# Kernel optimization log

Measured on AMD Instinct MI355X. Metric: run time of the kernel, lower is better.

Reference implementation:

```python
import jax, jax.numpy as jnp
import numpy as np

N_NODES = 50000


def gcn_conv(x, W, b, src, dst, n_nodes):
    # PyG GCNConv: h = D^{-1/2}(A+I)D^{-1/2} X W + b, with self-loops added.
    h = x @ W                                   # [N, H]
    loops = jnp.arange(n_nodes, dtype=src.dtype)
    s = jnp.concatenate([src, loops])           # [E+N]
    d = jnp.concatenate([dst, loops])
    deg = jax.ops.segment_sum(jnp.ones_like(d, dtype=h.dtype), d, num_segments=n_nodes)
    dinv = jnp.where(deg > 0, jax.lax.rsqrt(deg), 0.0)
    norm = dinv[s] * dinv[d]                    # [E+N]
    msg = h[s] * norm[:, None]                  # gather + scale
    agg = jax.ops.segment_sum(msg, d, num_segments=n_nodes)  # scatter-add
    return agg + b


def setup_inputs() -> dict:
    key = jax.random.key(0)
    ks = jax.random.split(key, 8)
    N, E, D, H, ED = N_NODES, 800000, 64, 64, 16
    sc = lambda f_in: 1.0 / np.sqrt(f_in)
    return {
        "x": jax.random.normal(ks[0], (N, D), dtype=jnp.float32),
        "src": jax.random.randint(ks[1], (E,), 0, N),
        "dst": jax.random.randint(ks[2], (E,), 0, N),
        "edge_attr": jax.random.normal(ks[3], (E, ED), dtype=jnp.float32),
        "W1": jax.random.normal(ks[4], (D, H), dtype=jnp.float32) * sc(D),
        "b1": jnp.zeros((H,), dtype=jnp.float32),
        "Wm1": jax.random.normal(ks[5], (2 * H + ED, H), dtype=jnp.float32) * sc(2 * H + ED),
        "bm1": jnp.zeros((H,), dtype=jnp.float32),
        "Wm2": jax.random.normal(ks[6], (H, 1), dtype=jnp.float32) * sc(H),
        "bm2": jnp.zeros((1,), dtype=jnp.float32),
    }


def reference(x, src, dst, edge_attr, W1, b1, Wm1, bm1, Wm2, bm2):
    h = jax.nn.relu(gcn_conv(x, W1, b1, src, dst, N_NODES))  # [N, H]
    edge_repr = jnp.concatenate([h[src], h[dst], edge_attr], axis=1)  # [E, 2H+ED]
    hidden = jax.nn.relu(edge_repr @ Wm1 + bm1)
    scores = jax.nn.sigmoid(hidden @ Wm2 + bm2)
    return scores.squeeze(-1)
```

## Files before the change

kernel.cpp:

```cpp
#include <hip/hip_runtime.h>
#include <math.h>


typedef __attribute__((ext_vector_type(8))) short bf16x8;
typedef __attribute__((ext_vector_type(4))) float f32x4;

#define MAXDEG 64
#define BSHIFT 7
#define BMASK 127
#define NBUCK 391
#define CAP 2560
#define CHUNK 4096
#define BINB 196
#define BPB 40

__device__ __forceinline__ unsigned short f2b(float f) {
    unsigned u = __float_as_uint(f);
    unsigned r = (u + 0x7FFFu + ((u >> 16) & 1u)) >> 16;
    return (unsigned short)r;
}

__global__ void __launch_bounds__(256) bin_pack(
        const int* __restrict__ dst, const int* __restrict__ src,
        unsigned int* __restrict__ region, int* __restrict__ gcur, int E,
        const float* __restrict__ Wm1, unsigned short* __restrict__ Bp) {
    __shared__ __align__(16) char smem[32768];
    const int bid = blockIdx.x, tid = threadIdx.x;

    if (bid < BINB) {
        int* lc = (int*)smem;
        int* s0 = lc + 512;
        int* s1 = s0 + 512;
        int* gb = s1 + 512;
        unsigned* lval = (unsigned*)(gb + 512);
        unsigned short* lbuk = (unsigned short*)(lval + 4096);

        for (int i = tid; i < 512; i += 256) lc[i] = 0;
        __syncthreads();

        unsigned kb[16], kv[16];
#pragma unroll
        for (int j = 0; j < 4; ++j) {
            int i4 = bid * 1024 + j * 256 + tid;
            bool ok = (i4 * 4 < E);
            int4 d4 = make_int4(0, 0, 0, 0), s4 = make_int4(0, 0, 0, 0);
            if (ok) { d4 = ((const int4*)dst)[i4]; s4 = ((const int4*)src)[i4]; }
            int dd[4] = {d4.x, d4.y, d4.z, d4.w};
            int ss[4] = {s4.x, s4.y, s4.z, s4.w};
#pragma unroll
            for (int k = 0; k < 4; ++k) {
                int idx = j * 4 + k;
                kb[idx] = 0xFFFFFFFFu;
                if (ok) {
                    int b = dd[k] >> BSHIFT;
                    int r = atomicAdd(&lc[b], 1);
                    kb[idx] = ((unsigned)b << 12) | (unsigned)r;
                    kv[idx] = ((unsigned)(dd[k] & BMASK) << 16) | (unsigned)ss[k];
                }
            }
        }
        __syncthreads();

        for (int i = tid; i < 512; i += 256) s0[i] = lc[i];
        __syncthreads();
        int* pin = s0; int* pout = s1;
        for (int off = 1; off < 512; off <<= 1) {
            for (int i = tid; i < 512; i += 256) {
                int v = pin[i];
                if (i >= off) v += pin[i - off];
                pout[i] = v;
            }
            __syncthreads();
            int* t = pin; pin = pout; pout = t;
        }
        int* lb = pout;
        for (int i = tid; i < 512; i += 256) lb[i] = pin[i] - lc[i];
        for (int i = tid; i < NBUCK; i += 256) {
            int c = lc[i];
            gb[i] = c ? atomicAdd(&gcur[i], c) : 0;
        }
        __syncthreads();

#pragma unroll
        for (int idx = 0; idx < 16; ++idx) {
            if (kb[idx] != 0xFFFFFFFFu) {
                int b = (int)(kb[idx] >> 12), r = (int)(kb[idx] & 4095u);
                int pos = lb[b] + r;
                lval[pos] = kv[idx];
                lbuk[pos] = (unsigned short)b;
            }
        }
        __syncthreads();

        int ne = E - bid * CHUNK; if (ne > CHUNK) ne = CHUNK;
        for (int i = tid; i < ne; i += 256) {
            int b = lbuk[i];
            int idx = gb[b] + (i - lb[b]);
            if (idx < CAP) region[(size_t)b * CAP + idx] = lval[i];
        }
    } else {
        int idx = (bid - BINB) * 256 + tid;
        if (idx < 10240) {
            int j = idx & 7, ln = (idx >> 3) & 63, t = (idx >> 9) & 3, s = idx >> 11;
            int k = s * 32 + (ln >> 4) * 8 + j, col = t * 16 + (ln & 15);
            float v = (k < 144) ? Wm1[k * 64 + col] : 0.0f;
            Bp[idx] = f2b(v);
        }
    }
}

__global__ void __launch_bounds__(256) build_csr(
        const unsigned int* __restrict__ region, const int* __restrict__ gcur,
        int* __restrict__ cnt, unsigned short* __restrict__ csr_pad, int N) {
    __shared__ unsigned short lcsr[128 * MAXDEG];
    __shared__ int lcnt[128];
    int b = blockIdx.x, tid = threadIdx.x;
    if (tid < 128) lcnt[tid] = 0;
    __syncthreads();
    int ecnt = gcur[b]; if (ecnt > CAP) ecnt = CAP;
    const unsigned int* reg = region + (size_t)b * CAP;
    for (int i = tid; i < ecnt; i += 256) {
        unsigned v = reg[i];
        int dloc = (int)(v >> 16), s = (int)(v & 0xFFFFu);
        int r = atomicAdd(&lcnt[dloc], 1);
        if (r < MAXDEG) lcsr[dloc * MAXDEG + r] = (unsigned short)s;
    }
    __syncthreads();
    int n0 = b << BSHIFT;
    int nb = N - n0; if (nb > 128) nb = 128;
    if (tid < nb) cnt[n0 + tid] = lcnt[tid];
    int4* gout = (int4*)(csr_pad + (size_t)n0 * MAXDEG);
    const int4* lin = (const int4*)lcsr;
    int tot = nb * 8;
    for (int i = tid; i < tot; i += 256) gout[i] = lin[i];
}

__global__ void __launch_bounds__(256) node_gemm_mfma(
        const float* __restrict__ x, const float* __restrict__ W1,
        const int* __restrict__ cnt, unsigned short* __restrict__ gbf, int NWT) {
    __shared__ unsigned short sB[4096];
    for (int i = threadIdx.x; i < 4096; i += 256) {
        int j = i & 7, ln = (i >> 3) & 63, t = (i >> 9) & 3, s = i >> 11;
        int k = s * 32 + (ln >> 4) * 8 + j, col = t * 16 + (ln & 15);
        sB[i] = f2b(W1[k * 64 + col]);
    }
    __syncthreads();
    int wid = blockIdx.x * 4 + (threadIdx.x >> 6);
    if (wid >= NWT) return;
    int lane = threadIdx.x & 63, m = lane & 15, quad = lane >> 4;
    int r0 = wid * 16;
    f32x4 acc[4];
#pragma unroll
    for (int t = 0; t < 4; ++t) acc[t] = (f32x4){0.f, 0.f, 0.f, 0.f};
    const bf16x8* bp = (const bf16x8*)sB;
#pragma unroll
    for (int s = 0; s < 2; ++s) {
        const float4* xp = (const float4*)(x + (size_t)(r0 + m) * 64 + s * 32 + quad * 8);
        float4 v0 = xp[0], v1 = xp[1];
        bf16x8 a;
        a[0] = (short)f2b(v0.x); a[1] = (short)f2b(v0.y);
        a[2] = (short)f2b(v0.z); a[3] = (short)f2b(v0.w);
        a[4] = (short)f2b(v1.x); a[5] = (short)f2b(v1.y);
        a[6] = (short)f2b(v1.z); a[7] = (short)f2b(v1.w);
#pragma unroll
        for (int t = 0; t < 4; ++t)
            acc[t] = __builtin_amdgcn_mfma_f32_16x16x32_bf16(
                a, bp[(s * 4 + t) * 64 + lane], acc[t], 0, 0, 0);
    }
#pragma unroll
    for (int reg = 0; reg < 4; ++reg) {
        int row = r0 + quad * 4 + reg;
        float di = rsqrtf((float)cnt[row] + 1.0f);
#pragma unroll
        for (int t = 0; t < 4; ++t)
            gbf[(size_t)row * 64 + t * 16 + m] = f2b(acc[t][reg] * di);
    }
}

#define ACC8(U) \
    a0 += __uint_as_float((unsigned)(U).x << 16); \
    a1 += __uint_as_float((unsigned)(U).x & 0xffff0000u); \
    a2 += __uint_as_float((unsigned)(U).y << 16); \
    a3 += __uint_as_float((unsigned)(U).y & 0xffff0000u); \
    a4 += __uint_as_float((unsigned)(U).z << 16); \
    a5 += __uint_as_float((unsigned)(U).z & 0xffff0000u); \
    a6 += __uint_as_float((unsigned)(U).w << 16); \
    a7 += __uint_as_float((unsigned)(U).w & 0xffff0000u);

__global__ void __launch_bounds__(256) gather_finalize(
        const unsigned short* __restrict__ gbf, const unsigned short* __restrict__ csr_pad,
        const int* __restrict__ cnt, const float* __restrict__ b1,
        unsigned short* __restrict__ hbf, int N) {
    int t = blockIdx.x * 256 + threadIdx.x;
    int node = t >> 3;
    if (node >= N) return;
    int c8 = t & 7;
    int deg = cnt[node];
    if (deg > MAXDEG) deg = MAXDEG;
    size_t base = (size_t)node << 6;
    const int4* gb4 = (const int4*)gbf;
    float a0 = 0.f, a1 = 0.f, a2 = 0.f, a3 = 0.f,
          a4 = 0.f, a5 = 0.f, a6 = 0.f, a7 = 0.f;
    int j = 0;
    for (; j + 4 <= deg; j += 4) {
        int s0 = (int)csr_pad[base + j];
        int s1 = (int)csr_pad[base + j + 1];
        int s2 = (int)csr_pad[base + j + 2];
        int s3 = (int)csr_pad[base + j + 3];
        int4 u0 = gb4[(size_t)s0 * 8 + c8];
        int4 u1 = gb4[(size_t)s1 * 8 + c8];
        int4 u2 = gb4[(size_t)s2 * 8 + c8];
        int4 u3 = gb4[(size_t)s3 * 8 + c8];
        ACC8(u0) ACC8(u1) ACC8(u2) ACC8(u3)
    }
    for (; j < deg; ++j) {
        int s0 = (int)csr_pad[base + j];
        int4 u0 = gb4[(size_t)s0 * 8 + c8];
        ACC8(u0)
    }
    {
        int4 u = gb4[(size_t)node * 8 + c8];
        ACC8(u)
    }
    float dd = rsqrtf((float)deg + 1.0f);
    const float4* bv = (const float4*)(b1 + c8 * 8);
    float4 b0 = bv[0], b14 = bv[1];
    float h0 = dd * a0 + b0.x,  h1 = dd * a1 + b0.y;
    float h2 = dd * a2 + b0.z,  h3 = dd * a3 + b0.w;
    float h4 = dd * a4 + b14.x, h5 = dd * a5 + b14.y;
    float h6 = dd * a6 + b14.z, h7 = dd * a7 + b14.w;
    h0 = h0 > 0.f ? h0 : 0.f; h1 = h1 > 0.f ? h1 : 0.f;
    h2 = h2 > 0.f ? h2 : 0.f; h3 = h3 > 0.f ? h3 : 0.f;
    h4 = h4 > 0.f ? h4 : 0.f; h5 = h5 > 0.f ? h5 : 0.f;
    h6 = h6 > 0.f ? h6 : 0.f; h7 = h7 > 0.f ? h7 : 0.f;
    int4 w;
    w.x = (int)((unsigned)f2b(h0) | ((unsigned)f2b(h1) << 16));
    w.y = (int)((unsigned)f2b(h2) | ((unsigned)f2b(h3) << 16));
    w.z = (int)((unsigned)f2b(h4) | ((unsigned)f2b(h5) << 16));
    w.w = (int)((unsigned)f2b(h6) | ((unsigned)f2b(h7) << 16));
    ((int4*)hbf)[(size_t)node * 8 + c8] = w;
}

__global__ void __launch_bounds__(256, 8) edge_mlp_mfma(
        const unsigned short* __restrict__ hbf, const float* __restrict__ ea,
        const int* __restrict__ src, const int* __restrict__ dst,
        const unsigned short* __restrict__ Bp,
        const float* __restrict__ bm1, const float* __restrict__ Wm2,
        const float* __restrict__ bm2, float* __restrict__ out, int E) {
    __shared__ unsigned short sB[10240];
    {
        const int4* gB = (const int4*)Bp;
        int4* lB = (int4*)sB;
#pragma unroll
        for (int i = 0; i < 5; ++i)
            lB[threadIdx.x + i * 256] = gB[threadIdx.x + i * 256];
    }
    __syncthreads();
    int lane = threadIdx.x & 63;
    int wave = threadIdx.x >> 6;
    int m = lane & 15, quad = lane >> 4;
    int e0 = (blockIdx.x * 4 + wave) * 16;
    if (e0 >= E) return;
    int e = e0 + m;
    int ec = e < E ? e : E - 1;
    int si = src[ec], di = dst[ec];
    bf16x8 af[5];
    af[0] = *(const bf16x8*)(hbf + (size_t)si * 64 + quad * 8);
    af[1] = *(const bf16x8*)(hbf + (size_t)si * 64 + 32 + quad * 8);
    af[2] = *(const bf16x8*)(hbf + (size_t)di * 64 + quad * 8);
    af[3] = *(const bf16x8*)(hbf + (size_t)di * 64 + 32 + quad * 8);
    if (quad < 2) {
        const float4* ep = (const float4*)(ea + (size_t)ec * 16 + quad * 8);
        float4 v0 = ep[0], v1 = ep[1];
        af[4][0] = (short)f2b(v0.x); af[4][1] = (short)f2b(v0.y);
        af[4][2] = (short)f2b(v0.z); af[4][3] = (short)f2b(v0.w);
        af[4][4] = (short)f2b(v1.x); af[4][5] = (short)f2b(v1.y);
        af[4][6] = (short)f2b(v1.z); af[4][7] = (short)f2b(v1.w);
    } else {
#pragma unroll
        for (int j = 0; j < 8; ++j) af[4][j] = 0;
    }
    __builtin_amdgcn_sched_barrier(0);
    f32x4 acc[4];
#pragma unroll
    for (int t = 0; t < 4; ++t) acc[t] = (f32x4){0.f, 0.f, 0.f, 0.f};
    const bf16x8* bp = (const bf16x8*)sB;
#pragma unroll
    for (int s = 0; s < 5; ++s) {
#pragma unroll
        for (int t = 0; t < 4; ++t)
            acc[t] = __builtin_amdgcn_mfma_f32_16x16x32_bf16(
                af[s], bp[(s * 4 + t) * 64 + lane], acc[t], 0, 0, 0);
    }
    float w2[4], bb[4];
#pragma unroll
    for (int t = 0; t < 4; ++t) {
        int col = t * 16 + m;
        bb[t] = bm1[col];
        w2[t] = Wm2[col];
    }
    float pr[4];
#pragma unroll
    for (int r = 0; r < 4; ++r) {
        float sum = 0.0f;
#pragma unroll
        for (int t = 0; t < 4; ++t) {
            float hv = acc[t][r] + bb[t];
            sum += (hv > 0.0f ? hv : 0.0f) * w2[t];
        }
        pr[r] = sum;
    }
#pragma unroll
    for (int off = 1; off < 16; off <<= 1) {
#pragma unroll
        for (int r = 0; r < 4; ++r) pr[r] += __shfl_xor(pr[r], off, 64);
    }
    float b2 = bm2[0];
    if (m < 4) {
        int eo = e0 + quad * 4 + m;
        if (eo < E) out[eo] = 1.0f / (1.0f + __expf(-(pr[m] + b2)));
    }
}

extern "C" void kernel_launch(void* const* d_in, const int* in_sizes, int n_in,
                              void* d_out, int out_size, void* d_ws, size_t ws_size,
                              hipStream_t stream) {
    const float* x   = (const float*)d_in[0];
    const int*   src = (const int*)d_in[1];
    const int*   dst = (const int*)d_in[2];
    const float* ea  = (const float*)d_in[3];
    const float* W1  = (const float*)d_in[4];
    const float* b1  = (const float*)d_in[5];
    const float* Wm1 = (const float*)d_in[6];
    const float* bm1 = (const float*)d_in[7];
    const float* Wm2 = (const float*)d_in[8];
    const float* bm2 = (const float*)d_in[9];
    float* out = (float*)d_out;

    int N = in_sizes[0] / 64;
    int E = in_sizes[1];
    int NWT = N / 16;

    char* p = (char*)d_ws;
    unsigned short* gbf     = (unsigned short*)p; p += (size_t)N * 64 * 2;
    unsigned short* hbf     = (unsigned short*)p; p += (size_t)N * 64 * 2;
    unsigned short* csr_pad = (unsigned short*)p; p += (size_t)N * MAXDEG * 2;
    int*            cnt     = (int*)p;            p += (size_t)N * 4;
    int*            gcur    = (int*)p;            p += (size_t)((NBUCK * 4 + 15) / 16) * 16;
    unsigned short* Bp      = (unsigned short*)p; p += 10240 * 2;
    unsigned int*   region  = (unsigned int*)hbf;

    hipMemsetAsync(gcur, 0, NBUCK * sizeof(int), stream);
    bin_pack<<<BINB + BPB, 256, 0, stream>>>(dst, src, region, gcur, E, Wm1, Bp);
    build_csr<<<NBUCK, 256, 0, stream>>>(region, gcur, cnt, csr_pad, N);
    node_gemm_mfma<<<(NWT + 3) / 4, 256, 0, stream>>>(x, W1, cnt, gbf, NWT);
    gather_finalize<<<(N * 8 + 255) / 256, 256, 0, stream>>>(gbf, csr_pad, cnt, b1, hbf, N);
    edge_mlp_mfma<<<(E + 63) / 64, 256, 0, stream>>>(hbf, ea, src, dst, Bp,
                                                     bm1, Wm2, bm2, out, E);
}
```

Before: 189.0 us.

## Drop CSR build; aggregate directly from bucketed edges via LDS atomics

Removes the build_csr kernel and padded CSR buffer. Degree counting moves into the node GEMM kernel, which reads bucket regions per 64-node half. Aggregation now runs one block per 128-node bucket and scatters gathered bf16 rows into a shared fp32 tile with LDS float atomics. bin_pack is also reconfigured with half-size chunks and twice the blocks. This saves one kernel launch and the CSR write/read, but adds many LDS atomics and a second pass over the region in gemm_cnt. It also drops the MAXDEG cap, which changes semantics for high-degree nodes, and region no longer aliases hbf.

```diff
diff --git a/kernel.cpp b/kernel.cpp
--- a/kernel.cpp
+++ b/kernel.cpp
@@ -10,9 +10,10 @@
 #define BMASK 127
 #define NBUCK 391
 #define CAP 2560
-#define CHUNK 4096
-#define BINB 196
+#define CHUNK 2048
+#define BINB 391
 #define BPB 40
+#define TSTR 68
 
 __device__ __forceinline__ unsigned short f2b(float f) {
     unsigned u = __float_as_uint(f);
@@ -24,7 +25,7 @@
         const int* __restrict__ dst, const int* __restrict__ src,
         unsigned int* __restrict__ region, int* __restrict__ gcur, int E,
         const float* __restrict__ Wm1, unsigned short* __restrict__ Bp) {
-    __shared__ __align__(16) char smem[32768];
+    __shared__ __align__(16) char smem[20480];
     const int bid = blockIdx.x, tid = threadIdx.x;
 
     if (bid < BINB) {
@@ -33,15 +34,15 @@
         int* s1 = s0 + 512;
         int* gb = s1 + 512;
         unsigned* lval = (unsigned*)(gb + 512);
-        unsigned short* lbuk = (unsigned short*)(lval + 4096);
+        unsigned short* lbuk = (unsigned short*)(lval + 2048);
 
         for (int i = tid; i < 512; i += 256) lc[i] = 0;
         __syncthreads();
 
-        unsigned kb[16], kv[16];
-#pragma unroll
-        for (int j = 0; j < 4; ++j) {
-            int i4 = bid * 1024 + j * 256 + tid;
+        unsigned kb[8], kv[8];
+#pragma unroll
+        for (int j = 0; j < 2; ++j) {
+            int i4 = bid * 512 + j * 256 + tid;
             bool ok = (i4 * 4 < E);
             int4 d4 = make_int4(0, 0, 0, 0), s4 = make_int4(0, 0, 0, 0);
             if (ok) { d4 = ((const int4*)dst)[i4]; s4 = ((const int4*)src)[i4]; }
@@ -82,7 +83,7 @@
         __syncthreads();
 
 #pragma unroll
-        for (int idx = 0; idx < 16; ++idx) {
+        for (int idx = 0; idx < 8; ++idx) {
             if (kb[idx] != 0xFFFFFFFFu) {
                 int b = (int)(kb[idx] >> 12), r = (int)(kb[idx] & 4095u);
                 int pos = lb[b] + r;
@@ -109,45 +110,35 @@
     }
 }
 
-__global__ void __launch_bounds__(256) build_csr(
+__global__ void __launch_bounds__(256) gemm_cnt(
+        const float* __restrict__ x, const float* __restrict__ W1,
         const unsigned int* __restrict__ region, const int* __restrict__ gcur,
-        int* __restrict__ cnt, unsigned short* __restrict__ csr_pad, int N) {
-    __shared__ unsigned short lcsr[128 * MAXDEG];
-    __shared__ int lcnt[128];
-    int b = blockIdx.x, tid = threadIdx.x;
-    if (tid < 128) lcnt[tid] = 0;
-    __syncthreads();
-    int ecnt = gcur[b]; if (ecnt > CAP) ecnt = CAP;
-    const unsigned int* reg = region + (size_t)b * CAP;
-    for (int i = tid; i < ecnt; i += 256) {
-        unsigned v = reg[i];
-        int dloc = (int)(v >> 16), s = (int)(v & 0xFFFFu);
-        int r = atomicAdd(&lcnt[dloc], 1);
-        if (r < MAXDEG) lcsr[dloc * MAXDEG + r] = (unsigned short)s;
-    }
-    __syncthreads();
-    int n0 = b << BSHIFT;
-    int nb = N - n0; if (nb > 128) nb = 128;
-    if (tid < nb) cnt[n0 + tid] = lcnt[tid];
-    int4* gout = (int4*)(csr_pad + (size_t)n0 * MAXDEG);
-    const int4* lin = (const int4*)lcsr;
-    int tot = nb * 8;
-    for (int i = tid; i < tot; i += 256) gout[i] = lin[i];
-}
-
-__global__ void __launch_bounds__(256) node_gemm_mfma(
-        const float* __restrict__ x, const float* __restrict__ W1,
-        const int* __restrict__ cnt, unsigned short* __restrict__ gbf, int NWT) {
+        unsigned short* __restrict__ gbf, int N) {
     __shared__ unsigned short sB[4096];
-    for (int i = threadIdx.x; i < 4096; i += 256) {
+    __shared__ int lcnt[64];
+    __shared__ float ldinv[64];
+    const int tid = threadIdx.x, bid = blockIdx.x;
+    for (int i = tid; i < 4096; i += 256) {
         int j = i & 7, ln = (i >> 3) & 63, t = (i >> 9) & 3, s = i >> 11;
         int k = s * 32 + (ln >> 4) * 8 + j, col = t * 16 + (ln & 15);
         sB[i] = f2b(W1[k * 64 + col]);
     }
-    __syncthreads();
-    int wid = blockIdx.x * 4 + (threadIdx.x >> 6);
+    if (tid < 64) lcnt[tid] = 0;
+    __syncthreads();
+    int bucket = bid >> 1, half = bid & 1;
+    int ecnt = gcur[bucket]; if (ecnt > CAP) ecnt = CAP;
+    const unsigned int* reg = region + (size_t)bucket * CAP;
+    for (int i = tid; i < ecnt; i += 256) {
+        int dloc = (int)(reg[i] >> 16);
+        if ((dloc >> 6) == half) atomicAdd(&lcnt[dloc & 63], 1);
+    }
+    __syncthreads();
+    if (tid < 64) ldinv[tid] = rsqrtf((float)lcnt[tid] + 1.0f);
+    __syncthreads();
+    int wid = bid * 4 + (tid >> 6);
+    int NWT = (N + 15) / 16;
     if (wid >= NWT) return;
-    int lane = threadIdx.x & 63, m = lane & 15, quad = lane >> 4;
+    int lane = tid & 63, m = lane & 15, quad = lane >> 4;
     int r0 = wid * 16;
     f32x4 acc[4];
 #pragma unroll
@@ -168,77 +159,84 @@
                 a, bp[(s * 4 + t) * 64 + lane], acc[t], 0, 0, 0);
     }
 #pragma unroll
-    for (int reg = 0; reg < 4; ++reg) {
-        int row = r0 + quad * 4 + reg;
-        float di = rsqrtf((float)cnt[row] + 1.0f);
+    for (int reg2 = 0; reg2 < 4; ++reg2) {
+        int row = r0 + quad * 4 + reg2;
+        float di = ldinv[row - bid * 64];
 #pragma unroll
         for (int t = 0; t < 4; ++t)
-            gbf[(size_t)row * 64 + t * 16 + m] = f2b(acc[t][reg] * di);
-    }
-}
-
-#define ACC8(U) \
-    a0 += __uint_as_float((unsigned)(U).x << 16); \
-    a1 += __uint_as_float((unsigned)(U).x & 0xffff0000u); \
-    a2 += __uint_as_float((unsigned)(U).y << 16); \
-    a3 += __uint_as_float((unsigned)(U).y & 0xffff0000u); \
-    a4 += __uint_as_float((unsigned)(U).z << 16); \
-    a5 += __uint_as_float((unsigned)(U).z & 0xffff0000u); \
-    a6 += __uint_as_float((unsigned)(U).w << 16); \
-    a7 += __uint_as_float((unsigned)(U).w & 0xffff0000u);
-
-__global__ void __launch_bounds__(256) gather_finalize(
-        const unsigned short* __restrict__ gbf, const unsigned short* __restrict__ csr_pad,
-        const int* __restrict__ cnt, const float* __restrict__ b1,
+            gbf[(size_t)row * 64 + t * 16 + m] = f2b(acc[t][reg2] * di);
+    }
+}
+
+__global__ void __launch_bounds__(256) aggregate_finalize(
+        const unsigned short* __restrict__ gbf, const unsigned int* __restrict__ region,
+        const int* __restrict__ gcur, const float* __restrict__ b1,
         unsigned short* __restrict__ hbf, int N) {
-    int t = blockIdx.x * 256 + threadIdx.x;
-    int node = t >> 3;
-    if (node >= N) return;
-    int c8 = t & 7;
-    int deg = cnt[node];
-    if (deg > MAXDEG) deg = MAXDEG;
-    size_t base = (size_t)node << 6;
+    __shared__ float tile[128 * TSTR];
+    __shared__ int lcnt[128];
+    const int tid = threadIdx.x, b = blockIdx.x;
+    {
+        float4* t4 = (float4*)tile;
+        for (int i = tid; i < 128 * TSTR / 4; i += 256)
+            t4[i] = make_float4(0.f, 0.f, 0.f, 0.f);
+    }
+    if (tid < 128) lcnt[tid] = 0;
+    __syncthreads();
+    int ecnt = gcur[b]; if (ecnt > CAP) ecnt = CAP;
+    const unsigned int* reg = region + (size_t)b * CAP;
     const int4* gb4 = (const int4*)gbf;
-    float a0 = 0.f, a1 = 0.f, a2 = 0.f, a3 = 0.f,
-          a4 = 0.f, a5 = 0.f, a6 = 0.f, a7 = 0.f;
-    int j = 0;
-    for (; j + 4 <= deg; j += 4) {
-        int s0 = (int)csr_pad[base + j];
-        int s1 = (int)csr_pad[base + j + 1];
-        int s2 = (int)csr_pad[base + j + 2];
-        int s3 = (int)csr_pad[base + j + 3];
-        int4 u0 = gb4[(size_t)s0 * 8 + c8];
-        int4 u1 = gb4[(size_t)s1 * 8 + c8];
-        int4 u2 = gb4[(size_t)s2 * 8 + c8];
-        int4 u3 = gb4[(size_t)s3 * 8 + c8];
-        ACC8(u0) ACC8(u1) ACC8(u2) ACC8(u3)
-    }
-    for (; j < deg; ++j) {
-        int s0 = (int)csr_pad[base + j];
-        int4 u0 = gb4[(size_t)s0 * 8 + c8];
-        ACC8(u0)
-    }
-    {
-        int4 u = gb4[(size_t)node * 8 + c8];
-        ACC8(u)
-    }
-    float dd = rsqrtf((float)deg + 1.0f);
-    const float4* bv = (const float4*)(b1 + c8 * 8);
-    float4 b0 = bv[0], b14 = bv[1];
-    float h0 = dd * a0 + b0.x,  h1 = dd * a1 + b0.y;
-    float h2 = dd * a2 + b0.z,  h3 = dd * a3 + b0.w;
-    float h4 = dd * a4 + b14.x, h5 = dd * a5 + b14.y;
-    float h6 = dd * a6 + b14.z, h7 = dd * a7 + b14.w;
-    h0 = h0 > 0.f ? h0 : 0.f; h1 = h1 > 0.f ? h1 : 0.f;
-    h2 = h2 > 0.f ? h2 : 0.f; h3 = h3 > 0.f ? h3 : 0.f;
-    h4 = h4 > 0.f ? h4 : 0.f; h5 = h5 > 0.f ? h5 : 0.f;
-    h6 = h6 > 0.f ? h6 : 0.f; h7 = h7 > 0.f ? h7 : 0.f;
-    int4 w;
-    w.x = (int)((unsigned)f2b(h0) | ((unsigned)f2b(h1) << 16));
-    w.y = (int)((unsigned)f2b(h2) | ((unsigned)f2b(h3) << 16));
-    w.z = (int)((unsigned)f2b(h4) | ((unsigned)f2b(h5) << 16));
-    w.w = (int)((unsigned)f2b(h6) | ((unsigned)f2b(h7) << 16));
-    ((int4*)hbf)[(size_t)node * 8 + c8] = w;
+    int ntask = ecnt * 8;
+    int c8 = tid & 7;
+    for (int i = tid; i < ntask; i += 256) {
+        int e = i >> 3;
+        unsigned v = reg[e];
+        int dloc = (int)(v >> 16), s = (int)(v & 0xFFFFu);
+        int4 u = gb4[(size_t)s * 8 + c8];
+        float* tr = &tile[dloc * TSTR + c8 * 8];
+        atomicAdd(&tr[0], __uint_as_float((unsigned)u.x << 16));
+        atomicAdd(&tr[1], __uint_as_float((unsigned)u.x & 0xffff0000u));
+        atomicAdd(&tr[2], __uint_as_float((unsigned)u.y << 16));
+        atomicAdd(&tr[3], __uint_as_float((unsigned)u.y & 0xffff0000u));
+        atomicAdd(&tr[4], __uint_as_float((unsigned)u.z << 16));
+        atomicAdd(&tr[5], __uint_as_float((unsigned)u.z & 0xffff0000u));
+        atomicAdd(&tr[6], __uint_as_float((unsigned)u.w << 16));
+        atomicAdd(&tr[7], __uint_as_float((unsigned)u.w & 0xffff0000u));
+        if (c8 == 0) atomicAdd(&lcnt[dloc], 1);
+    }
+    __syncthreads();
+    int n0 = b << BSHIFT;
+    int nb = N - n0; if (nb > 128) nb = 128;
+    for (int i = tid; i < nb * 8; i += 256) {
+        int dloc = i >> 3, cc = i & 7;
+        int node = n0 + dloc;
+        float dd = rsqrtf((float)lcnt[dloc] + 1.0f);
+        int4 u = gb4[(size_t)node * 8 + cc];
+        const float* tr = &tile[dloc * TSTR + cc * 8];
+        float a0 = tr[0] + __uint_as_float((unsigned)u.x << 16);
+        float a1 = tr[1] + __uint_as_float((unsigned)u.x & 0xffff0000u);
+        float a2 = tr[2] + __uint_as_float((unsigned)u.y << 16);
+        float a3 = tr[3] + __uint_as_float((unsigned)u.y & 0xffff0000u);
+        float a4 = tr[4] + __uint_as_float((unsigned)u.z << 16);
+        float a5 = tr[5] + __uint_as_float((unsigned)u.z & 0xffff0000u);
+        float a6 = tr[6] + __uint_as_float((unsigned)u.w << 16);
+        float a7 = tr[7] + __uint_as_float((unsigned)u.w & 0xffff0000u);
+        const float4* bv = (const float4*)(b1 + cc * 8);
+        float4 b0 = bv[0], b14 = bv[1];
+        float h0 = dd * a0 + b0.x,  h1 = dd * a1 + b0.y;
+        float h2 = dd * a2 + b0.z,  h3 = dd * a3 + b0.w;
+        float h4 = dd * a4 + b14.x, h5 = dd * a5 + b14.y;
+        float h6 = dd * a6 + b14.z, h7 = dd * a7 + b14.w;
+        h0 = h0 > 0.f ? h0 : 0.f; h1 = h1 > 0.f ? h1 : 0.f;
+        h2 = h2 > 0.f ? h2 : 0.f; h3 = h3 > 0.f ? h3 : 0.f;
+        h4 = h4 > 0.f ? h4 : 0.f; h5 = h5 > 0.f ? h5 : 0.f;
+        h6 = h6 > 0.f ? h6 : 0.f; h7 = h7 > 0.f ? h7 : 0.f;
+        int4 w;
+        w.x = (int)((unsigned)f2b(h0) | ((unsigned)f2b(h1) << 16));
+        w.y = (int)((unsigned)f2b(h2) | ((unsigned)f2b(h3) << 16));
+        w.z = (int)((unsigned)f2b(h4) | ((unsigned)f2b(h5) << 16));
+        w.w = (int)((unsigned)f2b(h6) | ((unsigned)f2b(h7) << 16));
+        ((int4*)hbf)[(size_t)node * 8 + cc] = w;
+    }
 }
 
 __global__ void __launch_bounds__(256, 8) edge_mlp_mfma(
@@ -339,22 +337,18 @@
 
     int N = in_sizes[0] / 64;
     int E = in_sizes[1];
-    int NWT = N / 16;
 
     char* p = (char*)d_ws;
-    unsigned short* gbf     = (unsigned short*)p; p += (size_t)N * 64 * 2;
-    unsigned short* hbf     = (unsigned short*)p; p += (size_t)N * 64 * 2;
-    unsigned short* csr_pad = (unsigned short*)p; p += (size_t)N * MAXDEG * 2;
-    int*            cnt     = (int*)p;            p += (size_t)N * 4;
-    int*            gcur    = (int*)p;            p += (size_t)((NBUCK * 4 + 15) / 16) * 16;
-    unsigned short* Bp      = (unsigned short*)p; p += 10240 * 2;
-    unsigned int*   region  = (unsigned int*)hbf;
+    unsigned short* gbf    = (unsigned short*)p; p += (size_t)N * 64 * 2;
+    unsigned short* hbf    = (unsigned short*)p; p += (size_t)N * 64 * 2;
+    unsigned int*   region = (unsigned int*)p;   p += (size_t)NBUCK * CAP * 4;
+    int*            gcur   = (int*)p;            p += (size_t)((NBUCK * 4 + 15) / 16) * 16;
+    unsigned short* Bp     = (unsigned short*)p; p += 10240 * 2;
 
     hipMemsetAsync(gcur, 0, NBUCK * sizeof(int), stream);
     bin_pack<<<BINB + BPB, 256, 0, stream>>>(dst, src, region, gcur, E, Wm1, Bp);
-    build_csr<<<NBUCK, 256, 0, stream>>>(region, gcur, cnt, csr_pad, N);
-    node_gemm_mfma<<<(NWT + 3) / 4, 256, 0, stream>>>(x, W1, cnt, gbf, NWT);
-    gather_finalize<<<(N * 8 + 255) / 256, 256, 0, stream>>>(gbf, csr_pad, cnt, b1, hbf, N);
+    gemm_cnt<<<(N + 63) / 64, 256, 0, stream>>>(x, W1, region, gcur, gbf, N);
+    aggregate_finalize<<<NBUCK, 256, 0, stream>>>(gbf, region, gcur, b1, hbf, N);
     edge_mlp_mfma<<<(E + 63) / 64, 256, 0, stream>>>(hbf, ea, src, dst, Bp,
                                                      bm1, Wm2, bm2, out, E);
 }
```

New measurement: 521.2 us. +175.7%, slower.

## Merge node GEMM into binning launch and defer degree scaling to CSR build

Applied to the files above, without the earlier changes.

The node X·W1 MFMA GEMM now runs as extra blocks inside the binning kernel, so it no longer needs the degree counts and no longer waits on its own launch. The D^-1/2 source scaling moves into the CSR build kernel, which rescales each bucket's 128 gbf rows in place once the counts are known. This drops one kernel launch and lets the GEMM overlap with edge binning. The cost is an extra read-modify-write pass over gbf and a second bf16 rounding of the scaled values.

```diff
diff --git a/kernel.cpp b/kernel.cpp
--- a/kernel.cpp
+++ b/kernel.cpp
@@ -12,6 +12,7 @@
 #define CAP 2560
 #define CHUNK 4096
 #define BINB 196
+#define GEMB 782
 #define BPB 40
 
 __device__ __forceinline__ unsigned short f2b(float f) {
@@ -20,10 +21,12 @@
     return (unsigned short)r;
 }
 
-__global__ void __launch_bounds__(256) bin_pack(
+__global__ void __launch_bounds__(256) bin_gemm_pack(
         const int* __restrict__ dst, const int* __restrict__ src,
         unsigned int* __restrict__ region, int* __restrict__ gcur, int E,
-        const float* __restrict__ Wm1, unsigned short* __restrict__ Bp) {
+        const float* __restrict__ x, const float* __restrict__ W1,
+        unsigned short* __restrict__ gbf,
+        const float* __restrict__ Wm1, unsigned short* __restrict__ Bp, int N) {
     __shared__ __align__(16) char smem[32768];
     const int bid = blockIdx.x, tid = threadIdx.x;
 
@@ -98,8 +101,47 @@
             int idx = gb[b] + (i - lb[b]);
             if (idx < CAP) region[(size_t)b * CAP + idx] = lval[i];
         }
+    } else if (bid < BINB + GEMB) {
+        unsigned short* sB = (unsigned short*)smem;
+        for (int i = tid; i < 4096; i += 256) {
+            int j = i & 7, ln = (i >> 3) & 63, t = (i >> 9) & 3, s = i >> 11;
+            int k = s * 32 + (ln >> 4) * 8 + j, col = t * 16 + (ln & 15);
+            sB[i] = f2b(W1[k * 64 + col]);
+        }
+        __syncthreads();
+        int wid = (bid - BINB) * 4 + (tid >> 6);
+        int NWT = N / 16;
+        if (wid < NWT) {
+            int lane = tid & 63, m = lane & 15, quad = lane >> 4;
+            int r0 = wid * 16;
+            f32x4 acc[4];
+#pragma unroll
+            for (int t = 0; t < 4; ++t) acc[t] = (f32x4){0.f, 0.f, 0.f, 0.f};
+            const bf16x8* bp = (const bf16x8*)sB;
+#pragma unroll
+            for (int s = 0; s < 2; ++s) {
+                const float4* xp = (const float4*)(x + (size_t)(r0 + m) * 64 + s * 32 + quad * 8);
+                float4 v0 = xp[0], v1 = xp[1];
+                bf16x8 a;
+                a[0] = (short)f2b(v0.x); a[1] = (short)f2b(v0.y);
+                a[2] = (short)f2b(v0.z); a[3] = (short)f2b(v0.w);
+                a[4] = (short)f2b(v1.x); a[5] = (short)f2b(v1.y);
+                a[6] = (short)f2b(v1.z); a[7] = (short)f2b(v1.w);
+#pragma unroll
+                for (int t = 0; t < 4; ++t)
+                    acc[t] = __builtin_amdgcn_mfma_f32_16x16x32_bf16(
+                        a, bp[(s * 4 + t) * 64 + lane], acc[t], 0, 0, 0);
+            }
+#pragma unroll
+            for (int reg = 0; reg < 4; ++reg) {
+                int row = r0 + quad * 4 + reg;
+#pragma unroll
+                for (int t = 0; t < 4; ++t)
+                    gbf[(size_t)row * 64 + t * 16 + m] = f2b(acc[t][reg]);
+            }
+        }
     } else {
-        int idx = (bid - BINB) * 256 + tid;
+        int idx = (bid - BINB - GEMB) * 256 + tid;
         if (idx < 10240) {
             int j = idx & 7, ln = (idx >> 3) & 63, t = (idx >> 9) & 3, s = idx >> 11;
             int k = s * 32 + (ln >> 4) * 8 + j, col = t * 16 + (ln & 15);
@@ -109,11 +151,13 @@
     }
 }
 
-__global__ void __launch_bounds__(256) build_csr(
+__global__ void __launch_bounds__(256) build_scale(
         const unsigned int* __restrict__ region, const int* __restrict__ gcur,
-        int* __restrict__ cnt, unsigned short* __restrict__ csr_pad, int N) {
+        int* __restrict__ cnt, unsigned short* __restrict__ csr_pad,
+        unsigned short* __restrict__ gbf, int N) {
     __shared__ unsigned short lcsr[128 * MAXDEG];
     __shared__ int lcnt[128];
+    __shared__ float ldinv[128];
     int b = blockIdx.x, tid = threadIdx.x;
     if (tid < 128) lcnt[tid] = 0;
     __syncthreads();
@@ -129,51 +173,32 @@
     int n0 = b << BSHIFT;
     int nb = N - n0; if (nb > 128) nb = 128;
     if (tid < nb) cnt[n0 + tid] = lcnt[tid];
-    int4* gout = (int4*)(csr_pad + (size_t)n0 * MAXDEG);
-    const int4* lin = (const int4*)lcsr;
-    int tot = nb * 8;
-    for (int i = tid; i < tot; i += 256) gout[i] = lin[i];
-}
-
-__global__ void __launch_bounds__(256) node_gemm_mfma(
-        const float* __restrict__ x, const float* __restrict__ W1,
-        const int* __restrict__ cnt, unsigned short* __restrict__ gbf, int NWT) {
-    __shared__ unsigned short sB[4096];
-    for (int i = threadIdx.x; i < 4096; i += 256) {
-        int j = i & 7, ln = (i >> 3) & 63, t = (i >> 9) & 3, s = i >> 11;
-        int k = s * 32 + (ln >> 4) * 8 + j, col = t * 16 + (ln & 15);
-        sB[i] = f2b(W1[k * 64 + col]);
+    if (tid < 128) ldinv[tid] = rsqrtf((float)lcnt[tid] + 1.0f);
+    {
+        int4* gout = (int4*)(csr_pad + (size_t)n0 * MAXDEG);
+        const int4* lin = (const int4*)lcsr;
+        int tot = nb * 8;
+        for (int i = tid; i < tot; i += 256) gout[i] = lin[i];
     }
     __syncthreads();
-    int wid = blockIdx.x * 4 + (threadIdx.x >> 6);
-    if (wid >= NWT) return;
-    int lane = threadIdx.x & 63, m = lane & 15, quad = lane >> 4;
-    int r0 = wid * 16;
-    f32x4 acc[4];
-#pragma unroll
-    for (int t = 0; t < 4; ++t) acc[t] = (f32x4){0.f, 0.f, 0.f, 0.f};
-    const bf16x8* bp = (const bf16x8*)sB;
-#pragma unroll
-    for (int s = 0; s < 2; ++s) {
-        const float4* xp = (const float4*)(x + (size_t)(r0 + m) * 64 + s * 32 + quad * 8);
-        float4 v0 = xp[0], v1 = xp[1];
-        bf16x8 a;
-        a[0] = (short)f2b(v0.x); a[1] = (short)f2b(v0.y);
-        a[2] = (short)f2b(v0.z); a[3] = (short)f2b(v0.w);
-        a[4] = (short)f2b(v1.x); a[5] = (short)f2b(v1.y);
-        a[6] = (short)f2b(v1.z); a[7] = (short)f2b(v1.w);
-#pragma unroll
-        for (int t = 0; t < 4; ++t)
-            acc[t] = __builtin_amdgcn_mfma_f32_16x16x32_bf16(
-                a, bp[(s * 4 + t) * 64 + lane], acc[t], 0, 0, 0);
-    }
-#pragma unroll
-    for (int reg = 0; reg < 4; ++reg) {
-        int row = r0 + quad * 4 + reg;
-        float di = rsqrtf((float)cnt[row] + 1.0f);
-#pragma unroll
-        for (int t = 0; t < 4; ++t)
-            gbf[(size_t)row * 64 + t * 16 + m] = f2b(acc[t][reg] * di);
+    int4* g4 = (int4*)(gbf + (size_t)n0 * 64);
+    for (int i = tid; i < nb * 8; i += 256) {
+        float di = ldinv[i >> 3];
+        int4 u = g4[i];
+        float f0 = __uint_as_float((unsigned)u.x << 16) * di;
+        float f1 = __uint_as_float((unsigned)u.x & 0xffff0000u) * di;
+        float f2 = __uint_as_float((unsigned)u.y << 16) * di;
+        float f3 = __uint_as_float((unsigned)u.y & 0xffff0000u) * di;
+        float f4 = __uint_as_float((unsigned)u.z << 16) * di;
+        float f5 = __uint_as_float((unsigned)u.z & 0xffff0000u) * di;
+        float f6 = __uint_as_float((unsigned)u.w << 16) * di;
+        float f7 = __uint_as_float((unsigned)u.w & 0xffff0000u) * di;
+        int4 w;
+        w.x = (int)((unsigned)f2b(f0) | ((unsigned)f2b(f1) << 16));
+        w.y = (int)((unsigned)f2b(f2) | ((unsigned)f2b(f3) << 16));
+        w.z = (int)((unsigned)f2b(f4) | ((unsigned)f2b(f5) << 16));
+        w.w = (int)((unsigned)f2b(f6) | ((unsigned)f2b(f7) << 16));
+        g4[i] = w;
     }
 }
 
@@ -339,7 +364,6 @@
 
     int N = in_sizes[0] / 64;
     int E = in_sizes[1];
-    int NWT = N / 16;
 
     char* p = (char*)d_ws;
     unsigned short* gbf     = (unsigned short*)p; p += (size_t)N * 64 * 2;
@@ -351,9 +375,9 @@
     unsigned int*   region  = (unsigned int*)hbf;
 
     hipMemsetAsync(gcur, 0, NBUCK * sizeof(int), stream);
-    bin_pack<<<BINB + BPB, 256, 0, stream>>>(dst, src, region, gcur, E, Wm1, Bp);
-    build_csr<<<NBUCK, 256, 0, stream>>>(region, gcur, cnt, csr_pad, N);
-    node_gemm_mfma<<<(NWT + 3) / 4, 256, 0, stream>>>(x, W1, cnt, gbf, NWT);
+    bin_gemm_pack<<<BINB + GEMB + BPB, 256, 0, stream>>>(
+        dst, src, region, gcur, E, x, W1, gbf, Wm1, Bp, N);
+    build_scale<<<NBUCK, 256, 0, stream>>>(region, gcur, cnt, csr_pad, gbf, N);
     gather_finalize<<<(N * 8 + 255) / 256, 256, 0, stream>>>(gbf, csr_pad, cnt, b1, hbf, N);
     edge_mlp_mfma<<<(E + 63) / 64, 256, 0, stream>>>(hbf, ea, src, dst, Bp,
                                                      bm1, Wm2, bm2, out, E);
```

After: 180.7 us. 4.4% less time.
